# Kernel tuning notes

Measured on AMD Instinct MI355X. Metric: run time of the kernel, lower is better.

Reference implementation:

```python
import jax, jax.numpy as jnp
import numpy as np

B, T, C = 4, 2048, 1024
H = 16
D = C // H  # head_dim = 64

def setup_inputs() -> dict:
    key = jax.random.key(0)
    k1, k2, k3 = jax.random.split(key, 3)
    x = jax.random.normal(k1, (B, T, C), dtype=jnp.float32)
    Wqkv = jax.random.normal(k2, (C, 3 * C), dtype=jnp.float32) * (C ** -0.5)
    Wproj = jax.random.normal(k3, (C, C), dtype=jnp.float32) * (C ** -0.5)
    return {"x": x, "Wqkv": Wqkv, "Wproj": Wproj}

def reference(x, Wqkv, Wproj):
    b, t, c = x.shape
    qkv = (x @ Wqkv).reshape(b, t, 3, H, D)
    qkv = jnp.transpose(qkv, (2, 0, 3, 1, 4))  # [3, B, H, T, D]
    q, k, v = qkv[0], qkv[1], qkv[2]
    att = jnp.einsum('bhqd,bhkd->bhqk', q, k) * (D ** -0.5)
    causal = jnp.tril(jnp.ones((t, t), dtype=bool))  # True where allowed
    att = jnp.where(causal, att, -jnp.inf)
    att = jax.nn.softmax(att, axis=-1)
    out = jnp.einsum('bhqk,bhkd->bhqd', att, v)  # [B, H, T, D]
    out = jnp.transpose(out, (0, 2, 1, 3)).reshape(b, t, c)
    return out @ Wproj
```

## Files before the change

kernel.cpp:

```cpp
#include <hip/hip_runtime.h>
#include <stdint.h>

typedef unsigned short u16;
typedef __bf16 bf16x8 __attribute__((ext_vector_type(8)));
typedef float f32x4 __attribute__((ext_vector_type(4)));

#define DEVI static __device__ __forceinline__

DEVI u16 f2bf(float f) {
  union { float f; unsigned u; } v; v.f = f;
  unsigned r = v.u + 0x7FFF + ((v.u >> 16) & 1);
  return (u16)(r >> 16);
}

DEVI unsigned pkbf(float a, float b) {
  union { float f; unsigned u; } x, y; x.f = a; y.f = b;
  return __builtin_amdgcn_perm(y.u + 0x8000u, x.u + 0x8000u, 0x07060302u);
}

DEVI void lds_fence() { asm volatile("s_waitcnt lgkmcnt(0)" ::: "memory"); }

DEVI void gl2lds16(const u16* g, u16* l) {
  __builtin_amdgcn_global_load_lds(
      (const __attribute__((address_space(1))) unsigned int*)(uintptr_t)g,
      (__attribute__((address_space(3))) unsigned int*)(uintptr_t)l,
      16, 0, 0);
}

__global__ __launch_bounds__(256)
void prep(const float* __restrict__ x, u16* __restrict__ xb,
          const float* __restrict__ Wqkv, u16* __restrict__ wqkvT,
          const float* __restrict__ Wproj, u16* __restrict__ wprojT) {
  __shared__ float tile[64][65];
  const int blk = blockIdx.x;
  if (blk < 8192) {
    const int i = blk * 256 + threadIdx.x;
    const float4 v = ((const float4*)x)[i];
    ushort4 o;
    o.x = f2bf(v.x); o.y = f2bf(v.y); o.z = f2bf(v.z); o.w = f2bf(v.w);
    ((ushort4*)xb)[i] = o;
    return;
  }
  const float* in; u16* out; int Cn, n0, r0;
  if (blk < 8960) {
    const int p = blk - 8192;
    in = Wqkv; out = wqkvT; Cn = 3072;
    n0 = (p % 48) * 64; r0 = (p / 48) * 64;
  } else {
    const int p = blk - 8960;
    in = Wproj; out = wprojT; Cn = 1024;
    n0 = (p % 16) * 64; r0 = (p / 16) * 64;
  }
#pragma unroll
  for (int i = 0; i < 16; ++i) {
    const int e = threadIdx.x + i * 256;
    const int r = e >> 6, c = e & 63;
    tile[r][c] = in[(size_t)(r0 + r) * Cn + n0 + c];
  }
  __syncthreads();
#pragma unroll
  for (int i = 0; i < 16; ++i) {
    const int e = threadIdx.x + i * 256;
    const int r = e >> 6, c = e & 63;
    out[(size_t)(n0 + r) * 1024 + r0 + c] = f2bf(tile[c][r]);
  }
}

template <int MODE>
__global__ __launch_bounds__(256)
void gemm128(const u16* __restrict__ A, const u16* __restrict__ Bt,
             int M, int N, int K, float* __restrict__ Cout,
             u16* __restrict__ Qg, u16* __restrict__ Kg, u16* __restrict__ Vtg) {
  __shared__ alignas(16) u16 As0[128 * 32];
  __shared__ alignas(16) u16 As1[128 * 32];
  __shared__ alignas(16) u16 Bs0[128 * 32];
  __shared__ alignas(16) u16 Bs1[128 * 32];
  const int tid = threadIdx.x;
  const int wave = tid >> 6, lane = tid & 63;
  const int quad = lane >> 4, l15 = lane & 15;
  const int m0 = blockIdx.y * 128;
  const int n0 = blockIdx.x * 128;
  const int wm = (wave >> 1) * 64;
  const int wn = (wave & 1) * 64;

  f32x4 acc[4][4] = {};

  const int q1 = wave * 64 + lane;
  const int q2 = q1 + 256;
  const int r1 = q1 >> 2, c1 = q1 & 3;
  const int r2 = q2 >> 2, c2 = q2 & 3;
  const size_t ga1 = (size_t)(m0 + r1) * K + c1 * 8;
  const size_t ga2 = (size_t)(m0 + r2) * K + c2 * 8;
  const size_t gb1 = (size_t)(n0 + r1) * K + c1 * 8;
  const size_t gb2 = (size_t)(n0 + r2) * K + c2 * 8;

  for (int k0 = 0; k0 < K; k0 += 64) {
    __syncthreads();
    gl2lds16(A + ga1 + k0, As0 + wave * 512);
    gl2lds16(A + ga2 + k0, As0 + 2048 + wave * 512);
    gl2lds16(Bt + gb1 + k0, Bs0 + wave * 512);
    gl2lds16(Bt + gb2 + k0, Bs0 + 2048 + wave * 512);
    gl2lds16(A + ga1 + k0 + 32, As1 + wave * 512);
    gl2lds16(A + ga2 + k0 + 32, As1 + 2048 + wave * 512);
    gl2lds16(Bt + gb1 + k0 + 32, Bs1 + wave * 512);
    gl2lds16(Bt + gb2 + k0 + 32, Bs1 + 2048 + wave * 512);
    __syncthreads();
#pragma unroll
    for (int kh = 0; kh < 2; ++kh) {
      const u16* Asl = kh ? As1 : As0;
      const u16* Bsl = kh ? Bs1 : Bs0;
      bf16x8 av[4], bv[4];
#pragma unroll
      for (int i = 0; i < 4; ++i)
        av[i] = *(const bf16x8*)(Asl + (wm + i * 16 + l15) * 32 + quad * 8);
#pragma unroll
      for (int j = 0; j < 4; ++j)
        bv[j] = *(const bf16x8*)(Bsl + (wn + j * 16 + l15) * 32 + quad * 8);
#pragma unroll
      for (int i = 0; i < 4; ++i)
#pragma unroll
        for (int j = 0; j < 4; ++j)
          acc[i][j] = __builtin_amdgcn_mfma_f32_16x16x32_bf16(av[i], bv[j], acc[i][j], 0, 0, 0);
    }
  }

  if constexpr (MODE == 0) {
#pragma unroll
    for (int i = 0; i < 4; ++i) {
#pragma unroll
      for (int j = 0; j < 4; ++j) {
        const int mb = m0 + wm + i * 16 + quad * 4;
        const int n = n0 + wn + j * 16 + l15;
#pragma unroll
        for (int r = 0; r < 4; ++r)
          Cout[(size_t)(mb + r) * N + n] = acc[i][j][r];
      }
    }
  } else {
    const int s0b = n0 >> 10;
    const int b = m0 >> 11;
    const int h = ((n0 + wn) >> 6) & 15;
    const int bh = b * 16 + h;
    const int tbase = (m0 & 2047) + wm;
    if (s0b == 2) {
      __syncthreads();
      u16* sl = (wave < 2 ? As0 : Bs0) + (wave & 1) * 2048;
#pragma unroll
      for (int jp = 0; jp < 2; ++jp) {
#pragma unroll
        for (int j2 = 0; j2 < 2; ++j2) {
          const int j = jp * 2 + j2;
          const int dl = j2 * 16 + l15;
          const int sw8 = dl & 7;
#pragma unroll
          for (int i = 0; i < 4; ++i) {
            const int tq = i * 2 + (quad >> 1);
            ushort4 pk;
            pk.x = f2bf(acc[i][j][0]); pk.y = f2bf(acc[i][j][1]);
            pk.z = f2bf(acc[i][j][2]); pk.w = f2bf(acc[i][j][3]);
            *(ushort4*)(sl + dl * 64 + ((tq ^ sw8) << 3) + (quad & 1) * 4) = pk;
          }
        }
        lds_fence();
#pragma unroll
        for (int p = 0; p < 4; ++p) {
          const int dl = p * 8 + (lane >> 3);
          const int tc = lane & 7;
          const int tcu = tc ^ (dl & 7);
          const uint4 v = *(const uint4*)(sl + dl * 64 + tc * 8);
          *(uint4*)(Vtg + ((size_t)(bh * 64 + jp * 32 + dl)) * 2048 + tbase + tcu * 8) = v;
        }
        lds_fence();
      }
    } else {
      u16* dst = s0b ? Kg : Qg;
      const float scale = s0b ? 1.0f : 0.18033688f;
#pragma unroll
      for (int i = 0; i < 4; ++i) {
        const int t0 = tbase + i * 16 + quad * 4;
#pragma unroll
        for (int j = 0; j < 4; ++j) {
          const int d = j * 16 + l15;
#pragma unroll
          for (int r = 0; r < 4; ++r)
            dst[((size_t)bh * 2048 + t0 + r) * 64 + d] = f2bf(acc[i][j][r] * scale);
        }
      }
    }
  }
}

__global__ __launch_bounds__(256)
void attn_fwd(const u16* __restrict__ Qg, const u16* __restrict__ Kg,
              const u16* __restrict__ Vtg, u16* __restrict__ Og) {
  __shared__ alignas(16) u16 Ks[64 * 64];
  __shared__ alignas(16) u16 Vts[64 * 64];
  __shared__ alignas(16) u16 Ps[4][2][16 * 64];

  const int tid = threadIdx.x;
  const int wave = tid >> 6, lane = tid & 63;
  const int quad = lane >> 4, l15 = lane & 15;
  const int bh = blockIdx.x & 63;
  const int qt = 15 - (blockIdx.x >> 6);
  const int b = bh >> 4, h = bh & 15;
  const int sw = l15 & 7;

  const int rs0 = wave * 16 + (lane >> 3);
  const int rs1 = rs0 + 8;
  const int cs = (lane & 7) ^ (rs0 & 7);
  const size_t kgb0 = (size_t)(bh * 2048 + rs0) * 64 + cs * 8;
  const size_t kgb1 = (size_t)(bh * 2048 + rs1) * 64 + cs * 8;
  const size_t vgb0 = (size_t)(bh * 64 + rs0) * 2048 + cs * 8;
  const size_t vgb1 = (size_t)(bh * 64 + rs1) * 2048 + cs * 8;
  const int ldsw0 = wave * 1024;
  const int ldsw1 = wave * 1024 + 512;

  const int qb0 = qt * 128 + wave * 32;

  bf16x8 bq[2][2];
#pragma unroll
  for (int qs = 0; qs < 2; ++qs)
#pragma unroll
    for (int hv = 0; hv < 2; ++hv)
      bq[qs][hv] = *(const bf16x8*)(Qg + ((size_t)bh * 2048 + qb0 + qs * 16 + l15) * 64 + hv * 32 + quad * 8);

  f32x4 oacc[2][4] = {};
  float li[2] = {0.f, 0.f};

  const int jlast = qt * 128 + 64;
  for (int j0 = 0; j0 <= jlast; j0 += 64) {
    __syncthreads();
    gl2lds16(Kg + kgb0 + (size_t)j0 * 64, Ks + ldsw0);
    gl2lds16(Kg + kgb1 + (size_t)j0 * 64, Ks + ldsw1);
    gl2lds16(Vtg + vgb0 + j0, Vts + ldsw0);
    gl2lds16(Vtg + vgb1 + j0, Vts + ldsw1);
    __syncthreads();
    if (j0 > qb0 + 31) continue;

    bf16x8 aK[4][2];
#pragma unroll
    for (int ks = 0; ks < 4; ++ks)
#pragma unroll
      for (int hv = 0; hv < 2; ++hv)
        aK[ks][hv] = *(const bf16x8*)(Ks + (ks * 16 + l15) * 64 + ((hv * 4 + quad) ^ sw) * 8);
    bf16x8 bV[4][2];
#pragma unroll
    for (int ds = 0; ds < 4; ++ds)
#pragma unroll
      for (int kc = 0; kc < 2; ++kc)
        bV[ds][kc] = *(const bf16x8*)(Vts + (ds * 16 + l15) * 64 + ((kc * 4 + quad) ^ sw) * 8);

#pragma unroll
    for (int qs = 0; qs < 2; ++qs) {
      const int qb = qb0 + qs * 16;
      if (j0 > qb + 15) continue;
      u16* Pw = Ps[wave][qs];
      const bool needmask = (j0 + 63 > qb);
#pragma unroll
      for (int ks = 0; ks < 4; ++ks) {
        f32x4 s = {};
        s = __builtin_amdgcn_mfma_f32_16x16x32_bf16(aK[ks][0], bq[qs][0], s, 0, 0, 0);
        s = __builtin_amdgcn_mfma_f32_16x16x32_bf16(aK[ks][1], bq[qs][1], s, 0, 0, 0);
        if (needmask) {
          const int kbase = j0 + ks * 16 + quad * 4;
          const int qrow = qb + l15;
#pragma unroll
          for (int r = 0; r < 4; ++r)
            if (kbase + r > qrow) s[r] = -1e30f;
        }
        float p0 = __builtin_amdgcn_exp2f(s[0]);
        float p1 = __builtin_amdgcn_exp2f(s[1]);
        float p2 = __builtin_amdgcn_exp2f(s[2]);
        float p3 = __builtin_amdgcn_exp2f(s[3]);
        li[qs] += (p0 + p1) + (p2 + p3);
        uint2 pk;
        pk.x = pkbf(p0, p1);
        pk.y = pkbf(p2, p3);
        *(uint2*)(Pw + l15 * 64 + (((ks * 2 + (quad >> 1)) ^ sw) * 8) + (quad & 1) * 4) = pk;
      }
      lds_fence();
      bf16x8 aP0 = *(const bf16x8*)(Pw + l15 * 64 + ((0 * 4 + quad) ^ sw) * 8);
      bf16x8 aP1 = *(const bf16x8*)(Pw + l15 * 64 + ((1 * 4 + quad) ^ sw) * 8);
#pragma unroll
      for (int ds = 0; ds < 4; ++ds) {
        oacc[qs][ds] = __builtin_amdgcn_mfma_f32_16x16x32_bf16(aP0, bV[ds][0], oacc[qs][ds], 0, 0, 0);
        oacc[qs][ds] = __builtin_amdgcn_mfma_f32_16x16x32_bf16(aP1, bV[ds][1], oacc[qs][ds], 0, 0, 0);
      }
    }
  }

#pragma unroll
  for (int qs = 0; qs < 2; ++qs) {
    float l = li[qs];
    l += __shfl_xor(l, 16);
    l += __shfl_xor(l, 32);
    const int qb = qb0 + qs * 16;
#pragma unroll
    for (int r = 0; r < 4; ++r) {
      const float lrow = __shfl(l, quad * 4 + r);
      const float inv = 1.0f / lrow;
      u16* orow = Og + ((size_t)b * 2048 + qb + quad * 4 + r) * 1024 + h * 64;
#pragma unroll
      for (int ds = 0; ds < 4; ++ds)
        orow[ds * 16 + l15] = f2bf(oacc[qs][ds][r] * inv);
    }
  }
}

extern "C" void kernel_launch(void* const* d_in, const int* in_sizes, int n_in,
                              void* d_out, int out_size, void* d_ws, size_t ws_size,
                              hipStream_t stream) {
  const float* x = (const float*)d_in[0];
  const float* Wqkv = (const float*)d_in[1];
  const float* Wproj = (const float*)d_in[2];
  float* out = (float*)d_out;

  char* ws = (char*)d_ws;
  u16* xb     = (u16*)(ws);
  u16* wqkvT  = (u16*)(ws + 16777216);
  u16* wprojT = (u16*)(ws + 23068672);
  u16* Qg     = (u16*)(ws + 25165824);
  u16* Kg     = (u16*)(ws + 41943040);
  u16* Vtg    = (u16*)(ws + 58720256);
  u16* Og     = (u16*)(ws + 75497472);

  prep<<<9216, 256, 0, stream>>>(x, xb, Wqkv, wqkvT, Wproj, wprojT);
  gemm128<1><<<dim3(24, 64), 256, 0, stream>>>(xb, wqkvT, 8192, 3072, 1024,
                                               nullptr, Qg, Kg, Vtg);
  attn_fwd<<<1024, 256, 0, stream>>>(Qg, Kg, Vtg, Og);
  gemm128<0><<<dim3(8, 64), 256, 0, stream>>>(Og, wprojT, 8192, 1024, 1024,
                                              out, nullptr, nullptr, nullptr);
}
```

Before: 245.8 us.

## Double-buffer K/V tiles in attention kernel to overlap loads with compute

Splits the K and V shared-memory tiles into two buffers so the next tile's global-to-LDS load is issued before computing on the current one. This replaces the two barriers per iteration with a single wait plus barrier at the end, hiding load latency. It also raises wave priority around the compute section and shares one P scratch buffer per wave across both query sub-blocks. The cost is more LDS per block, which could lower occupancy, and reusing the P buffer across sub-blocks relies on in-wave ordering of the LDS writes and reads.

Result: no change. 243.3 us (-1.0%).

```diff
diff --git a/kernel.cpp b/kernel.cpp
--- a/kernel.cpp
+++ b/kernel.cpp
@@ -193,9 +193,9 @@
 __global__ __launch_bounds__(256)
 void attn_fwd(const u16* __restrict__ Qg, const u16* __restrict__ Kg,
               const u16* __restrict__ Vtg, u16* __restrict__ Og) {
-  __shared__ alignas(16) u16 Ks[64 * 64];
-  __shared__ alignas(16) u16 Vts[64 * 64];
-  __shared__ alignas(16) u16 Ps[4][2][16 * 64];
+  __shared__ alignas(16) u16 Ks[2][64 * 64];
+  __shared__ alignas(16) u16 Vts[2][64 * 64];
+  __shared__ alignas(16) u16 Ps[4][16 * 64];
 
   const int tid = threadIdx.x;
   const int wave = tid >> 6, lane = tid & 63;
@@ -228,65 +228,85 @@
   float li[2] = {0.f, 0.f};
 
   const int jlast = qt * 128 + 64;
-  for (int j0 = 0; j0 <= jlast; j0 += 64) {
-    __syncthreads();
-    gl2lds16(Kg + kgb0 + (size_t)j0 * 64, Ks + ldsw0);
-    gl2lds16(Kg + kgb1 + (size_t)j0 * 64, Ks + ldsw1);
-    gl2lds16(Vtg + vgb0 + j0, Vts + ldsw0);
-    gl2lds16(Vtg + vgb1 + j0, Vts + ldsw1);
-    __syncthreads();
-    if (j0 > qb0 + 31) continue;
-
-    bf16x8 aK[4][2];
-#pragma unroll
-    for (int ks = 0; ks < 4; ++ks)
-#pragma unroll
-      for (int hv = 0; hv < 2; ++hv)
-        aK[ks][hv] = *(const bf16x8*)(Ks + (ks * 16 + l15) * 64 + ((hv * 4 + quad) ^ sw) * 8);
-    bf16x8 bV[4][2];
-#pragma unroll
-    for (int ds = 0; ds < 4; ++ds)
-#pragma unroll
-      for (int kc = 0; kc < 2; ++kc)
-        bV[ds][kc] = *(const bf16x8*)(Vts + (ds * 16 + l15) * 64 + ((kc * 4 + quad) ^ sw) * 8);
-
-#pragma unroll
-    for (int qs = 0; qs < 2; ++qs) {
-      const int qb = qb0 + qs * 16;
-      if (j0 > qb + 15) continue;
-      u16* Pw = Ps[wave][qs];
-      const bool needmask = (j0 + 63 > qb);
-#pragma unroll
-      for (int ks = 0; ks < 4; ++ks) {
-        f32x4 s = {};
-        s = __builtin_amdgcn_mfma_f32_16x16x32_bf16(aK[ks][0], bq[qs][0], s, 0, 0, 0);
-        s = __builtin_amdgcn_mfma_f32_16x16x32_bf16(aK[ks][1], bq[qs][1], s, 0, 0, 0);
-        if (needmask) {
-          const int kbase = j0 + ks * 16 + quad * 4;
-          const int qrow = qb + l15;
-#pragma unroll
-          for (int r = 0; r < 4; ++r)
-            if (kbase + r > qrow) s[r] = -1e30f;
-        }
-        float p0 = __builtin_amdgcn_exp2f(s[0]);
-        float p1 = __builtin_amdgcn_exp2f(s[1]);
-        float p2 = __builtin_amdgcn_exp2f(s[2]);
-        float p3 = __builtin_amdgcn_exp2f(s[3]);
-        li[qs] += (p0 + p1) + (p2 + p3);
-        uint2 pk;
-        pk.x = pkbf(p0, p1);
-        pk.y = pkbf(p2, p3);
-        *(uint2*)(Pw + l15 * 64 + (((ks * 2 + (quad >> 1)) ^ sw) * 8) + (quad & 1) * 4) = pk;
+  const int nt = (jlast >> 6) + 1;
+
+  gl2lds16(Kg + kgb0, Ks[0] + ldsw0);
+  gl2lds16(Kg + kgb1, Ks[0] + ldsw1);
+  gl2lds16(Vtg + vgb0, Vts[0] + ldsw0);
+  gl2lds16(Vtg + vgb1, Vts[0] + ldsw1);
+  asm volatile("s_waitcnt vmcnt(0)" ::: "memory");
+  __builtin_amdgcn_s_barrier();
+
+  for (int t = 0; t < nt; ++t) {
+    const int j0 = t << 6;
+    const int cur = t & 1;
+    if (t + 1 < nt) {
+      const size_t ko = (size_t)(j0 + 64) * 64;
+      gl2lds16(Kg + kgb0 + ko, Ks[cur ^ 1] + ldsw0);
+      gl2lds16(Kg + kgb1 + ko, Ks[cur ^ 1] + ldsw1);
+      gl2lds16(Vtg + vgb0 + j0 + 64, Vts[cur ^ 1] + ldsw0);
+      gl2lds16(Vtg + vgb1 + j0 + 64, Vts[cur ^ 1] + ldsw1);
+    }
+
+    if (j0 <= qb0 + 31) {
+      __builtin_amdgcn_s_setprio(1);
+      const u16* Kc = Ks[cur];
+      const u16* Vc = Vts[cur];
+      bf16x8 aK[4][2];
+#pragma unroll
+      for (int ks = 0; ks < 4; ++ks)
+#pragma unroll
+        for (int hv = 0; hv < 2; ++hv)
+          aK[ks][hv] = *(const bf16x8*)(Kc + (ks * 16 + l15) * 64 + ((hv * 4 + quad) ^ sw) * 8);
+      bf16x8 bV[4][2];
+#pragma unroll
+      for (int ds = 0; ds < 4; ++ds)
+#pragma unroll
+        for (int kc = 0; kc < 2; ++kc)
+          bV[ds][kc] = *(const bf16x8*)(Vc + (ds * 16 + l15) * 64 + ((kc * 4 + quad) ^ sw) * 8);
+
+#pragma unroll
+      for (int qs = 0; qs < 2; ++qs) {
+        const int qb = qb0 + qs * 16;
+        if (j0 > qb + 15) continue;
+        u16* Pw = Ps[wave];
+        const bool needmask = (j0 + 63 > qb);
+#pragma unroll
+        for (int ks = 0; ks < 4; ++ks) {
+          f32x4 s = {};
+          s = __builtin_amdgcn_mfma_f32_16x16x32_bf16(aK[ks][0], bq[qs][0], s, 0, 0, 0);
+          s = __builtin_amdgcn_mfma_f32_16x16x32_bf16(aK[ks][1], bq[qs][1], s, 0, 0, 0);
+          if (needmask) {
+            const int kbase = j0 + ks * 16 + quad * 4;
+            const int qrow = qb + l15;
+#pragma unroll
+            for (int r = 0; r < 4; ++r)
+              if (kbase + r > qrow) s[r] = -1e30f;
+          }
+          float p0 = __builtin_amdgcn_exp2f(s[0]);
+          float p1 = __builtin_amdgcn_exp2f(s[1]);
+          float p2 = __builtin_amdgcn_exp2f(s[2]);
+          float p3 = __builtin_amdgcn_exp2f(s[3]);
+          li[qs] += (p0 + p1) + (p2 + p3);
+          uint2 pk;
+          pk.x = pkbf(p0, p1);
+          pk.y = pkbf(p2, p3);
+          *(uint2*)(Pw + l15 * 64 + (((ks * 2 + (quad >> 1)) ^ sw) * 8) + (quad & 1) * 4) = pk;
+        }
+        lds_fence();
+        bf16x8 aP0 = *(const bf16x8*)(Pw + l15 * 64 + ((0 * 4 + quad) ^ sw) * 8);
+        bf16x8 aP1 = *(const bf16x8*)(Pw + l15 * 64 + ((1 * 4 + quad) ^ sw) * 8);
+#pragma unroll
+        for (int ds = 0; ds < 4; ++ds) {
+          oacc[qs][ds] = __builtin_amdgcn_mfma_f32_16x16x32_bf16(aP0, bV[ds][0], oacc[qs][ds], 0, 0, 0);
+          oacc[qs][ds] = __builtin_amdgcn_mfma_f32_16x16x32_bf16(aP1, bV[ds][1], oacc[qs][ds], 0, 0, 0);
+        }
       }
-      lds_fence();
-      bf16x8 aP0 = *(const bf16x8*)(Pw + l15 * 64 + ((0 * 4 + quad) ^ sw) * 8);
-      bf16x8 aP1 = *(const bf16x8*)(Pw + l15 * 64 + ((1 * 4 + quad) ^ sw) * 8);
-#pragma unroll
-      for (int ds = 0; ds < 4; ++ds) {
-        oacc[qs][ds] = __builtin_amdgcn_mfma_f32_16x16x32_bf16(aP0, bV[ds][0], oacc[qs][ds], 0, 0, 0);
-        oacc[qs][ds] = __builtin_amdgcn_mfma_f32_16x16x32_bf16(aP1, bV[ds][1], oacc[qs][ds], 0, 0, 0);
-      }
-    }
+      __builtin_amdgcn_s_setprio(0);
+    }
+
+    asm volatile("s_waitcnt vmcnt(0)" ::: "memory");
+    __builtin_amdgcn_s_barrier();
   }
 
 #pragma unroll
```
